# Performance work log

Hardware: AMD Instinct MI355X
Metric: run time of the kernel (lower is better)

The kernel has to match this reference:

```python
import jax, jax.numpy as jnp
import numpy as np

B, T, C = 2, 2048, 1024
NH = 16
HS = C // NH

def setup_inputs() -> dict:
    key = jax.random.key(0)
    ks = jax.random.split(key, 5)
    x = jax.random.normal(ks[0], (B, T, C), dtype=jnp.float32)
    scale = 1.0 / np.sqrt(C)
    Wk = jax.random.normal(ks[1], (C, C), dtype=jnp.float32) * scale
    bk = jax.random.normal(ks[2], (C,), dtype=jnp.float32) * scale
    Wv = jax.random.normal(ks[3], (C, C), dtype=jnp.float32) * scale
    bv = jax.random.normal(ks[4], (C,), dtype=jnp.float32) * scale
    return {"x": x, "Wk": Wk, "bk": bk, "Wv": Wv, "bv": bv}

def reference(x, Wk, bk, Wv, bv):
    b, t, c = x.shape
    # projections: key and value are Dense; query is identity (as in source)
    k = (x @ Wk + bk).reshape(b, t, NH, HS).transpose(0, 2, 1, 3)  # b nh T hs
    q = x.reshape(b, t, NH, HS).transpose(0, 2, 1, 3)              # b nh T hs
    v = (x @ Wv + bv).reshape(b, t, NH, HS).transpose(0, 2, 1, 3)  # b nh T hs
    # NOTE: source computes logits = K @ Q^T (no 1/sqrt(d) scaling)
    logits = jnp.einsum('bhid,bhjd->bhij', k, q)                   # b nh T T
    causal = jnp.tril(jnp.ones((t, t), dtype=bool))                # True where allowed
    masked = jnp.where(causal[None, None, :, :], logits, -jnp.inf)
    att = jax.nn.softmax(masked, axis=-1)
    y = jnp.einsum('bhij,bhjd->bhid', att, v)                      # b nh T hs
    return y.transpose(0, 2, 1, 3).reshape(b, t, c)
```

## Files before the change

kernel.cpp:

```cpp
#include <hip/hip_runtime.h>
#include <cstdint>
#include <cstddef>

#define BB  2
#define TT  2048
#define CC  1024
#define NHH 16
#define HSS 64
#define BT  (BB*TT)

#define LOG2E 1.44269504088896f
#define S0INIT (-28.8539008f)

typedef unsigned short u16;
typedef unsigned int u32;
typedef __attribute__((ext_vector_type(2))) unsigned int u32x2;
typedef _Float16 f16;
typedef __attribute__((ext_vector_type(8))) _Float16 f16x8;
typedef __attribute__((ext_vector_type(8))) __bf16 bf16x8;
typedef __attribute__((ext_vector_type(4))) float f32x4;

__device__ __forceinline__ u16 f2bf(float f) {
    union { float f; u32 u; } x; x.f = f;
    return (u16)((x.u + 0x7fffu + ((x.u >> 16) & 1u)) >> 16);
}
__device__ __forceinline__ u16 f2h(float f) {
    union { f16 h; u16 u; } x; x.h = (f16)f;
    return x.u;
}
__device__ __forceinline__ u32 cvtpk_bf16(float lo, float hi) {
    u32 r;
    asm("v_cvt_pk_bf16_f32 %0, %1, %2" : "=v"(r) : "v"(lo), "v"(hi));
    return r;
}

#define MFMA_BF(a,b,c) __builtin_amdgcn_mfma_f32_16x16x32_bf16((a),(b),(c),0,0,0)
#define MFMA_F16(a,b,c) __builtin_amdgcn_mfma_f32_16x16x32_f16((a),(b),(c),0,0,0)

__device__ __forceinline__ void gld16(const u16* g, u16* l) {
    __builtin_amdgcn_global_load_lds(
        (const __attribute__((address_space(1))) unsigned int*)g,
        (__attribute__((address_space(3))) unsigned int*)l, 16, 0, 0);
}

__global__ __launch_bounds__(256) void convert_xw(
    const float* __restrict__ X, const float* __restrict__ Wk,
    const float* __restrict__ Wv, u16* __restrict__ Xf,
    u16* __restrict__ WkT, u16* __restrict__ WvT)
{
    __shared__ __align__(16) u16 LH[64][72];
    const int bid = blockIdx.x;
    const int tid = threadIdx.x;
    if (bid < 2048) {
        const int idx = (bid * 256 + tid) * 8;
        const float4 a = *(const float4*)&X[idx];
        const float4 b = *(const float4*)&X[idx + 4];
        float v[8] = {a.x, a.y, a.z, a.w, b.x, b.y, b.z, b.w};
        union { uint4 u; u16 s[8]; } H;
        #pragma unroll
        for (int u = 0; u < 8; ++u) H.s[u] = f2h(v[u]);
        *(uint4*)&Xf[idx] = H.u;
        return;
    }
    const int bid2 = bid - 2048;
    const bool isK = (bid2 >> 8) == 0;
    const int rem = bid2 & 255;
    const int n0 = (rem & 15) * 64, k0 = (rem >> 4) * 64;
    const float* W = isK ? Wk : Wv;
    u16* WT = isK ? WkT : WvT;
    {
        const int row = tid >> 2, coff = (tid & 3) * 16;
        const float* g = &W[(size_t)(k0 + row) * CC + n0 + coff];
        #pragma unroll
        for (int u = 0; u < 16; ++u) LH[row][coff + u] = f2h(g[u]);
    }
    __syncthreads();
    {
        const int n = tid >> 2, kc = (tid & 3) * 16;
        union { uint4 u[2]; u16 s[16]; } Hq;
        #pragma unroll
        for (int u = 0; u < 16; ++u) Hq.s[u] = LH[kc + u][n];
        uint4* ph = (uint4*)&WT[(size_t)(n0 + n) * CC + k0 + kc];
        ph[0] = Hq.u[0]; ph[1] = Hq.u[1];
    }
}

__global__ __launch_bounds__(256) void proj_kernel(
    const u16* __restrict__ Xf, const u16* __restrict__ WkT,
    const u16* __restrict__ WvT,
    const float* __restrict__ bk, const float* __restrict__ bv,
    u16* __restrict__ Kf, u16* __restrict__ Vt)
{
    __shared__ __align__(16) u16 SM[4][8192];

    const int id = blockIdx.x;
    const int xcd = id & 7;
    const int z = xcd >> 2, xcd4 = xcd & 3;
    const int idx = id >> 3;
    const int n0 = (idx & 7) * 128;
    const int m0 = (xcd4 * 8 + (idx >> 3)) * 128;
    const bool isK = (z == 0);
    const u16* WT = isK ? WkT : WvT;

    const int tid = threadIdx.x;
    const int w = tid >> 6, lane = tid & 63;
    const int quad = lane >> 4, l15 = lane & 15;
    const int wm = (w >> 1) * 64, wn = (w & 1) * 64;

    const u16* src = (w < 2) ? Xf : WT;
    const int rbase = (w < 2) ? m0 : n0;
    int srow[4], scg[4];
    #pragma unroll
    for (int t = 0; t < 4; ++t) {
        const int ci = (w & 1) * 256 + t * 64 + lane;
        const int r = ci >> 2;
        srow[t] = r;
        scg[t] = ((ci & 3) - r - (r >> 2)) & 3;
    }
    const int dhalf = ((w >= 2) ? 4096 : 0) + (w & 1) * 2048;
    const u16* gsrc[4];
    #pragma unroll
    for (int t = 0; t < 4; ++t)
        gsrc[t] = src + (size_t)(rbase + srow[t]) * CC + scg[t] * 8;

    const char* smb = (const char*)&SM[0][0];
    int aoff[4], boff[4];
    #pragma unroll
    for (int i = 0; i < 4; ++i) {
        const int r = wm + i * 16 + l15;
        aoff[i] = r * 64 + ((quad + r + (r >> 2)) & 3) * 16;
    }
    #pragma unroll
    for (int j = 0; j < 4; ++j) {
        const int r = wn + j * 16 + l15;
        boff[j] = 8192 + r * 64 + ((quad + r + (r >> 2)) & 3) * 16;
    }

    f32x4 acc[4][4] = {};

#define PSTAGE(K, BI)                                                   \
    { u16* dst = &SM[BI][dhalf];                                        \
      _Pragma("unroll")                                                 \
      for (int t = 0; t < 4; ++t)                                       \
          gld16(gsrc[t] + (K) * 32, dst + t * 512); }

    PSTAGE(0, 0);
    PSTAGE(1, 1);

    for (int ki = 0; ki < 32; ++ki) {
        const int buf = ki & 3;
        if (ki < 30) PSTAGE(ki + 2, (ki + 2) & 3);
        if (ki < 30)       asm volatile("s_waitcnt vmcnt(8)" ::: "memory");
        else if (ki == 30) asm volatile("s_waitcnt vmcnt(4)" ::: "memory");
        else               asm volatile("s_waitcnt vmcnt(0)" ::: "memory");
        __builtin_amdgcn_sched_barrier(0);
        __builtin_amdgcn_s_barrier();
        __builtin_amdgcn_sched_barrier(0);
        const char* pb = smb + buf * 16384;
        f16x8 ah[4];
        #pragma unroll
        for (int i = 0; i < 4; ++i) ah[i] = *(const f16x8*)(pb + aoff[i]);
        #pragma unroll
        for (int j = 0; j < 4; ++j) {
            f16x8 bh = *(const f16x8*)(pb + boff[j]);
            #pragma unroll
            for (int i = 0; i < 4; ++i)
                acc[i][j] = MFMA_F16(ah[i], bh, acc[i][j]);
        }
    }
#undef PSTAGE

    __syncthreads();
    u16* XL = &SM[0][0];

    if (isK) {
        #pragma unroll
        for (int j = 0; j < 4; ++j) {
            const float bias = bk[n0 + wn + j * 16 + l15];
            #pragma unroll
            for (int i = 0; i < 4; ++i)
                #pragma unroll
                for (int r = 0; r < 4; ++r)
                    XL[(wm + i * 16 + quad * 4 + r) * 136 + wn + j * 16 + l15] =
                        f2h((acc[i][j][r] + bias) * LOG2E);
        }
        __syncthreads();
        const int r = tid >> 1, half = tid & 1;
        #pragma unroll
        for (int t = 0; t < 8; ++t)
            *(uint4*)&Kf[(size_t)(m0 + r) * CC + n0 + half * 64 + t * 8] =
                *(const uint4*)&XL[r * 136 + half * 64 + t * 8];
    } else {
        #pragma unroll
        for (int j = 0; j < 4; ++j) {
            const float bias = bv[n0 + wn + j * 16 + l15];
            #pragma unroll
            for (int i = 0; i < 4; ++i) {
                uint2 pk;
                pk.x = (u32)f2bf(acc[i][j][0] + bias) |
                       ((u32)f2bf(acc[i][j][1] + bias) << 16);
                pk.y = (u32)f2bf(acc[i][j][2] + bias) |
                       ((u32)f2bf(acc[i][j][3] + bias) << 16);
                *(uint2*)&XL[(wn + j * 16 + l15) * 136 + wm + i * 16 + quad * 4] = pk;
            }
        }
        __syncthreads();
        const int nl = tid >> 1, half = tid & 1;
        const int d = (n0 + nl) & (HSS - 1), hh = (n0 + nl) >> 6;
        const int bb = m0 >> 11, tb = (m0 & (TT - 1)) + half * 64;
        const size_t gb = ((size_t)(bb * NHH + hh) * HSS + d) * TT + tb;
        #pragma unroll
        for (int t = 0; t < 8; ++t)
            *(uint4*)&Vt[gb + t * 8] = *(const uint4*)&XL[nl * 136 + half * 64 + t * 8];
    }
}

__global__ __launch_bounds__(256) void attn_kernel(
    const u16* __restrict__ Xf, const u16* __restrict__ Kf,
    const u16* __restrict__ Vt, float* __restrict__ out)
{
    __shared__ __align__(16) u16 Xs[2][4096];
    __shared__ __align__(16) u16 Vs[2][4096];

    const int L = blockIdx.x;
    const int xcd = L & 7, k = (L >> 3) & 15, grp = L >> 7;
    const int hb = xcd + 8 * grp;
    const int h = hb & (NHH - 1), b = hb >> 4;
    const int iA = k, iB = 31 - k;
    const int i0A = iA * 64, i0B = iB * 64;

    const int tid = threadIdx.x;
    const int w = tid >> 6, lane = tid & 63;
    const int quad = lane >> 4, l15 = lane & 15;
    const int pq = ((quad & 1) << 1) | (quad >> 1);
    const size_t rowbase = (size_t)b * TT;
    const int hd = h * HSS;
    const size_t vgbase = (size_t)(b * NHH + h) * HSS * TT;

    bf16x8 ones;
    { union { u32 u[4]; bf16x8 v; } o;
      #pragma unroll
      for (int i = 0; i < 4; ++i) o.u[i] = 0x3F803F80u;
      ones = o.v; }

    f16x8 qA[2], qB[2];
    #pragma unroll
    for (int c = 0; c < 2; ++c) {
        qA[c] = *(const f16x8*)&Kf[(rowbase + i0A + w * 16 + l15) * CC + hd + c * 32 + quad * 8];
        qB[c] = *(const f16x8*)&Kf[(rowbase + i0B + w * 16 + l15) * CC + hd + c * 32 + quad * 8];
    }

    int crow[2], ccg[2], cbase[2];
    #pragma unroll
    for (int t = 0; t < 2; ++t) {
        const int ci = t * 256 + tid;
        crow[t] = ci >> 3;
        ccg[t] = ((ci & 7) - crow[t]) & 7;
        cbase[t] = (t * 256 + w * 64) * 8;
    }
    const u16* gx[2]; const u16* gv[2];
    #pragma unroll
    for (int t = 0; t < 2; ++t) {
        gx[t] = Xf + (rowbase + crow[t]) * CC + hd + ccg[t] * 8;
        gv[t] = Vt + vgbase + (size_t)crow[t] * TT + ccg[t] * 8;
    }

    #pragma unroll
    for (int t = 0; t < 2; ++t) {
        gld16(gx[t], Xs[0] + cbase[t]);
        gld16(gv[t], Vs[0] + cbase[t]);
    }

    f32x4 oA[4] = {}, oB[4] = {};
    f32x4 laA = {}, laB = {};

    for (int jt = 0; jt <= iB; ++jt) {
        const int buf = jt & 1;
        __syncthreads();
        if (jt < iB) {
            const int j0n = (jt + 1) * 64;
            #pragma unroll
            for (int t = 0; t < 2; ++t) {
                gld16(gx[t] + (size_t)j0n * CC, Xs[buf ^ 1] + cbase[t]);
                gld16(gv[t] + j0n, Vs[buf ^ 1] + cbase[t]);
            }
        }
        const bool doA = (jt <= iA);

        f32x4 sB[4], sA[4];
        #pragma unroll
        for (int nt = 0; nt < 4; ++nt) {
            const int krow = nt * 16 + l15;
            f16x8 x0 = *(const f16x8*)&Xs[buf][krow * 64 + ((quad + krow) & 7) * 8];
            f16x8 x1 = *(const f16x8*)&Xs[buf][krow * 64 + ((quad + 4 + krow) & 7) * 8];
            f32x4 z = {S0INIT, S0INIT, S0INIT, S0INIT};
            z = MFMA_F16(x0, qB[0], z);
            z = MFMA_F16(x1, qB[1], z);
            sB[nt] = z;
            if (doA) {
                f32x4 y = {S0INIT, S0INIT, S0INIT, S0INIT};
                y = MFMA_F16(x0, qA[0], y);
                y = MFMA_F16(x1, qA[1], y);
                sA[nt] = y;
            }
        }
        if (jt == iB) {
            #pragma unroll
            for (int nt = 0; nt < 4; ++nt)
                #pragma unroll
                for (int r = 0; r < 4; ++r)
                    if (nt * 16 + quad * 4 + r > w * 16 + l15) sB[nt][r] = -1e30f;
        }
        if (doA && jt == iA) {
            #pragma unroll
            for (int nt = 0; nt < 4; ++nt)
                #pragma unroll
                for (int r = 0; r < 4; ++r)
                    if (nt * 16 + quad * 4 + r > w * 16 + l15) sA[nt][r] = -1e30f;
        }

        u32 pB_[4][2];
        #pragma unroll
        for (int nt = 0; nt < 4; ++nt) {
            pB_[nt][0] = cvtpk_bf16(exp2f(sB[nt][0]), exp2f(sB[nt][1]));
            pB_[nt][1] = cvtpk_bf16(exp2f(sB[nt][2]), exp2f(sB[nt][3]));
        }
        #pragma unroll
        for (int c = 0; c < 2; ++c)
            #pragma unroll
            for (int p = 0; p < 2; ++p) {
                u32x2 sw = __builtin_amdgcn_permlane16_swap(
                    pB_[2 * c][p], pB_[2 * c + 1][p], false, false);
                pB_[2 * c][p] = sw[0];
                pB_[2 * c + 1][p] = sw[1];
            }
        union { u32 u[4]; bf16x8 v; } ub0, ub1;
        ub0.u[0] = pB_[0][0]; ub0.u[1] = pB_[0][1];
        ub0.u[2] = pB_[1][0]; ub0.u[3] = pB_[1][1];
        ub1.u[0] = pB_[2][0]; ub1.u[1] = pB_[2][1];
        ub1.u[2] = pB_[3][0]; ub1.u[3] = pB_[3][1];
        bf16x8 aB0 = ub0.v, aB1 = ub1.v;

        bf16x8 aA0, aA1;
        if (doA) {
            u32 pA_[4][2];
            #pragma unroll
            for (int nt = 0; nt < 4; ++nt) {
                pA_[nt][0] = cvtpk_bf16(exp2f(sA[nt][0]), exp2f(sA[nt][1]));
                pA_[nt][1] = cvtpk_bf16(exp2f(sA[nt][2]), exp2f(sA[nt][3]));
            }
            #pragma unroll
            for (int c = 0; c < 2; ++c)
                #pragma unroll
                for (int p = 0; p < 2; ++p) {
                    u32x2 sw = __builtin_amdgcn_permlane16_swap(
                        pA_[2 * c][p], pA_[2 * c + 1][p], false, false);
                    pA_[2 * c][p] = sw[0];
                    pA_[2 * c + 1][p] = sw[1];
                }
            union { u32 u[4]; bf16x8 v; } ua0, ua1;
            ua0.u[0] = pA_[0][0]; ua0.u[1] = pA_[0][1];
            ua0.u[2] = pA_[1][0]; ua0.u[3] = pA_[1][1];
            ua1.u[0] = pA_[2][0]; ua1.u[1] = pA_[2][1];
            ua1.u[2] = pA_[3][0]; ua1.u[3] = pA_[3][1];
            aA0 = ua0.v; aA1 = ua1.v;
        }

        laB = MFMA_BF(aB0, ones, laB);
        laB = MFMA_BF(aB1, ones, laB);
        if (doA) {
            laA = MFMA_BF(aA0, ones, laA);
            laA = MFMA_BF(aA1, ones, laA);
        }

        #pragma unroll
        for (int dt = 0; dt < 4; ++dt) {
            const int vrow = dt * 16 + l15;
            bf16x8 v0 = *(const bf16x8*)&Vs[buf][vrow * 64 + ((pq + vrow) & 7) * 8];
            bf16x8 v1 = *(const bf16x8*)&Vs[buf][vrow * 64 + ((pq + 4 + vrow) & 7) * 8];
            oB[dt] = MFMA_BF(aB0, v0, oB[dt]);
            oB[dt] = MFMA_BF(aB1, v1, oB[dt]);
            if (doA) {
                oA[dt] = MFMA_BF(aA0, v0, oA[dt]);
                oA[dt] = MFMA_BF(aA1, v1, oA[dt]);
            }
        }
    }

    float liA[4], liB[4];
    #pragma unroll
    for (int r = 0; r < 4; ++r) { liA[r] = 1.f / laA[r]; liB[r] = 1.f / laB[r]; }
    #pragma unroll
    for (int dt = 0; dt < 4; ++dt) {
        #pragma unroll
        for (int r = 0; r < 4; ++r) {
            const int igA = i0A + w * 16 + quad * 4 + r;
            const int igB = i0B + w * 16 + quad * 4 + r;
            out[(rowbase + igA) * CC + hd + dt * 16 + l15] = oA[dt][r] * liA[r];
            out[(rowbase + igB) * CC + hd + dt * 16 + l15] = oB[dt][r] * liB[r];
        }
    }
}

extern "C" void kernel_launch(void* const* d_in, const int* in_sizes, int n_in,
                              void* d_out, int out_size, void* d_ws, size_t ws_size,
                              hipStream_t stream) {
    (void)in_sizes; (void)n_in; (void)out_size; (void)ws_size;
    const float* x  = (const float*)d_in[0];
    const float* Wk = (const float*)d_in[1];
    const float* bk = (const float*)d_in[2];
    const float* Wv = (const float*)d_in[3];
    const float* bv = (const float*)d_in[4];
    float* out = (float*)d_out;

    const size_t M4 = (size_t)BT * CC;
    const size_t M1 = (size_t)CC * CC;
    u16* Xf  = (u16*)d_ws;
    u16* Kf  = Xf + M4;
    u16* Vt  = Kf + M4;
    u16* WkT = Vt + M4;
    u16* WvT = WkT + M1;

    convert_xw<<<dim3(2560), 256, 0, stream>>>(x, Wk, Wv, Xf, WkT, WvT);
    proj_kernel<<<dim3(512), 256, 0, stream>>>(Xf, WkT, WvT, bk, bv, Kf, Vt);
    attn_kernel<<<dim3(512), 256, 0, stream>>>(Xf, Kf, Vt, out);
}
```

Measured before the change: 154.2 us.

## Load K/V tiles directly from global into registers, dropping LDS double buffering

```diff
diff --git a/kernel.cpp b/kernel.cpp
--- a/kernel.cpp
+++ b/kernel.cpp
@@ -219,9 +219,6 @@
     const u16* __restrict__ Xf, const u16* __restrict__ Kf,
     const u16* __restrict__ Vt, float* __restrict__ out)
 {
-    __shared__ __align__(16) u16 Xs[2][4096];
-    __shared__ __align__(16) u16 Vs[2][4096];
-
     const int L = blockIdx.x;
     const int xcd = L & 7, k = (L >> 3) & 15, grp = L >> 7;
     const int hb = xcd + 8 * grp;
@@ -250,57 +247,46 @@
         qB[c] = *(const f16x8*)&Kf[(rowbase + i0B + w * 16 + l15) * CC + hd + c * 32 + quad * 8];
     }
 
-    int crow[2], ccg[2], cbase[2];
-    #pragma unroll
-    for (int t = 0; t < 2; ++t) {
-        const int ci = t * 256 + tid;
-        crow[t] = ci >> 3;
-        ccg[t] = ((ci & 7) - crow[t]) & 7;
-        cbase[t] = (t * 256 + w * 64) * 8;
-    }
-    const u16* gx[2]; const u16* gv[2];
-    #pragma unroll
-    for (int t = 0; t < 2; ++t) {
-        gx[t] = Xf + (rowbase + crow[t]) * CC + hd + ccg[t] * 8;
-        gv[t] = Vt + vgbase + (size_t)crow[t] * TT + ccg[t] * 8;
-    }
-
-    #pragma unroll
-    for (int t = 0; t < 2; ++t) {
-        gld16(gx[t], Xs[0] + cbase[t]);
-        gld16(gv[t], Vs[0] + cbase[t]);
+    const u16* xr[4];
+    const u16* vr[4];
+    #pragma unroll
+    for (int t = 0; t < 4; ++t) {
+        xr[t] = Xf + (rowbase + t * 16 + l15) * CC + hd + quad * 8;
+        vr[t] = Vt + vgbase + (size_t)(t * 16 + l15) * TT + pq * 8;
     }
 
     f32x4 oA[4] = {}, oB[4] = {};
     f32x4 laA = {}, laB = {};
 
     for (int jt = 0; jt <= iB; ++jt) {
-        const int buf = jt & 1;
-        __syncthreads();
-        if (jt < iB) {
-            const int j0n = (jt + 1) * 64;
-            #pragma unroll
-            for (int t = 0; t < 2; ++t) {
-                gld16(gx[t] + (size_t)j0n * CC, Xs[buf ^ 1] + cbase[t]);
-                gld16(gv[t] + j0n, Vs[buf ^ 1] + cbase[t]);
-            }
-        }
         const bool doA = (jt <= iA);
 
+        f16x8 x0[4], x1[4];
+        bf16x8 v0[4], v1[4];
+        #pragma unroll
+        for (int t = 0; t < 4; ++t) {
+            x0[t] = *(const f16x8*)(xr[t]);
+            x1[t] = *(const f16x8*)(xr[t] + 32);
+            v0[t] = *(const bf16x8*)(vr[t]);
+            v1[t] = *(const bf16x8*)(vr[t] + 32);
+        }
+        #pragma unroll
+        for (int t = 0; t < 4; ++t) {
+            xr[t] += 64 * CC;
+            vr[t] += 64;
+        }
+
         f32x4 sB[4], sA[4];
         #pragma unroll
         for (int nt = 0; nt < 4; ++nt) {
-            const int krow = nt * 16 + l15;
-            f16x8 x0 = *(const f16x8*)&Xs[buf][krow * 64 + ((quad + krow) & 7) * 8];
-            f16x8 x1 = *(const f16x8*)&Xs[buf][krow * 64 + ((quad + 4 + krow) & 7) * 8];
             f32x4 z = {S0INIT, S0INIT, S0INIT, S0INIT};
-            z = MFMA_F16(x0, qB[0], z);
-            z = MFMA_F16(x1, qB[1], z);
+            z = MFMA_F16(x0[nt], qB[0], z);
+            z = MFMA_F16(x1[nt], qB[1], z);
             sB[nt] = z;
             if (doA) {
                 f32x4 y = {S0INIT, S0INIT, S0INIT, S0INIT};
-                y = MFMA_F16(x0, qA[0], y);
-                y = MFMA_F16(x1, qA[1], y);
+                y = MFMA_F16(x0[nt], qA[0], y);
+                y = MFMA_F16(x1[nt], qA[1], y);
                 sA[nt] = y;
             }
         }
@@ -375,14 +361,11 @@
 
         #pragma unroll
         for (int dt = 0; dt < 4; ++dt) {
-            const int vrow = dt * 16 + l15;
-            bf16x8 v0 = *(const bf16x8*)&Vs[buf][vrow * 64 + ((pq + vrow) & 7) * 8];
-            bf16x8 v1 = *(const bf16x8*)&Vs[buf][vrow * 64 + ((pq + 4 + vrow) & 7) * 8];
-            oB[dt] = MFMA_BF(aB0, v0, oB[dt]);
-            oB[dt] = MFMA_BF(aB1, v1, oB[dt]);
+            oB[dt] = MFMA_BF(aB0, v0[dt], oB[dt]);
+            oB[dt] = MFMA_BF(aB1, v1[dt], oB[dt]);
             if (doA) {
-                oA[dt] = MFMA_BF(aA0, v0, oA[dt]);
-                oA[dt] = MFMA_BF(aA1, v1, oA[dt]);
+                oA[dt] = MFMA_BF(aA0, v0[dt], oA[dt]);
+                oA[dt] = MFMA_BF(aA1, v1[dt], oA[dt]);
             }
         }
     }
```

Result: slower. 222.1 us (+44.0%).

## Deepen attention K/V prefetch to 4-buffer, 2-ahead pipeline with explicit vmcnt waits

Applied to the files above, without the earlier changes.

```diff
diff --git a/kernel.cpp b/kernel.cpp
--- a/kernel.cpp
+++ b/kernel.cpp
@@ -219,8 +219,8 @@
     const u16* __restrict__ Xf, const u16* __restrict__ Kf,
     const u16* __restrict__ Vt, float* __restrict__ out)
 {
-    __shared__ __align__(16) u16 Xs[2][4096];
-    __shared__ __align__(16) u16 Vs[2][4096];
+    __shared__ __align__(16) u16 Xs[4][4096];
+    __shared__ __align__(16) u16 Vs[4][4096];
 
     const int L = blockIdx.x;
     const int xcd = L & 7, k = (L >> 3) & 15, grp = L >> 7;
@@ -265,26 +265,34 @@
         gv[t] = Vt + vgbase + (size_t)crow[t] * TT + ccg[t] * 8;
     }
 
-    #pragma unroll
-    for (int t = 0; t < 2; ++t) {
-        gld16(gx[t], Xs[0] + cbase[t]);
-        gld16(gv[t], Vs[0] + cbase[t]);
-    }
+#define ASTAGE(JT, BI)                                                  \
+    { const int j0_ = (JT) * 64;                                        \
+      _Pragma("unroll")                                                 \
+      for (int t = 0; t < 2; ++t) {                                     \
+          gld16(gx[t] + (size_t)j0_ * CC, Xs[BI] + cbase[t]);           \
+          gld16(gv[t] + j0_, Vs[BI] + cbase[t]);                        \
+      } }
+
+    ASTAGE(0, 0);
+    ASTAGE(1, 1);
 
     f32x4 oA[4] = {}, oB[4] = {};
     f32x4 laA = {}, laB = {};
 
     for (int jt = 0; jt <= iB; ++jt) {
-        const int buf = jt & 1;
-        __syncthreads();
-        if (jt < iB) {
-            const int j0n = (jt + 1) * 64;
-            #pragma unroll
-            for (int t = 0; t < 2; ++t) {
-                gld16(gx[t] + (size_t)j0n * CC, Xs[buf ^ 1] + cbase[t]);
-                gld16(gv[t] + j0n, Vs[buf ^ 1] + cbase[t]);
-            }
-        }
+        const int buf = jt & 3;
+        if (jt + 2 <= iB) {
+            ASTAGE(jt + 2, (jt + 2) & 3);
+            asm volatile("s_waitcnt vmcnt(8)" ::: "memory");
+        } else if (jt + 1 <= iB) {
+            asm volatile("s_waitcnt vmcnt(4)" ::: "memory");
+        } else {
+            asm volatile("s_waitcnt vmcnt(0)" ::: "memory");
+        }
+        __builtin_amdgcn_sched_barrier(0);
+        __builtin_amdgcn_s_barrier();
+        __builtin_amdgcn_sched_barrier(0);
+
         const bool doA = (jt <= iA);
 
         f32x4 sB[4], sA[4];
@@ -386,6 +394,7 @@
             }
         }
     }
+#undef ASTAGE
 
     float liA[4], liB[4];
     #pragma unroll
```

Result: no change. 155.6 us (+0.9%).

## Split attention work across warps by query tile and key half with LDS reduction

Applied to the files above, without the earlier changes.

```diff
diff --git a/kernel.cpp b/kernel.cpp
--- a/kernel.cpp
+++ b/kernel.cpp
@@ -221,16 +221,20 @@
 {
     __shared__ __align__(16) u16 Xs[2][4096];
     __shared__ __align__(16) u16 Vs[2][4096];
+    __shared__ float OL[2][64][65];
+    __shared__ float Ll[2][64];
 
     const int L = blockIdx.x;
     const int xcd = L & 7, k = (L >> 3) & 15, grp = L >> 7;
     const int hb = xcd + 8 * grp;
     const int h = hb & (NHH - 1), b = hb >> 4;
     const int iA = k, iB = 31 - k;
-    const int i0A = iA * 64, i0B = iB * 64;
-
     const int tid = threadIdx.x;
     const int w = tid >> 6, lane = tid & 63;
+    const int T = w >> 1;
+    const int H = w & 1;
+    const int iT = T ? iB : iA;
+    const int i0T = iT * 64;
     const int quad = lane >> 4, l15 = lane & 15;
     const int pq = ((quad & 1) << 1) | (quad >> 1);
     const size_t rowbase = (size_t)b * TT;
@@ -243,12 +247,13 @@
       for (int i = 0; i < 4; ++i) o.u[i] = 0x3F803F80u;
       ones = o.v; }
 
-    f16x8 qA[2], qB[2];
-    #pragma unroll
-    for (int c = 0; c < 2; ++c) {
-        qA[c] = *(const f16x8*)&Kf[(rowbase + i0A + w * 16 + l15) * CC + hd + c * 32 + quad * 8];
-        qB[c] = *(const f16x8*)&Kf[(rowbase + i0B + w * 16 + l15) * CC + hd + c * 32 + quad * 8];
-    }
+    f16x8 q[4][2];
+    #pragma unroll
+    for (int iq = 0; iq < 4; ++iq)
+        #pragma unroll
+        for (int c = 0; c < 2; ++c)
+            q[iq][c] = *(const f16x8*)&Kf[(rowbase + i0T + iq * 16 + l15) * CC +
+                                          hd + c * 32 + quad * 8];
 
     int crow[2], ccg[2], cbase[2];
     #pragma unroll
@@ -271,8 +276,8 @@
         gld16(gv[t], Vs[0] + cbase[t]);
     }
 
-    f32x4 oA[4] = {}, oB[4] = {};
-    f32x4 laA = {}, laB = {};
+    f32x4 o[4][4] = {};
+    f32x4 la[4] = {};
 
     for (int jt = 0; jt <= iB; ++jt) {
         const int buf = jt & 1;
@@ -285,119 +290,94 @@
                 gld16(gv[t] + j0n, Vs[buf ^ 1] + cbase[t]);
             }
         }
-        const bool doA = (jt <= iA);
-
-        f32x4 sB[4], sA[4];
-        #pragma unroll
-        for (int nt = 0; nt < 4; ++nt) {
-            const int krow = nt * 16 + l15;
-            f16x8 x0 = *(const f16x8*)&Xs[buf][krow * 64 + ((quad + krow) & 7) * 8];
-            f16x8 x1 = *(const f16x8*)&Xs[buf][krow * 64 + ((quad + 4 + krow) & 7) * 8];
-            f32x4 z = {S0INIT, S0INIT, S0INIT, S0INIT};
-            z = MFMA_F16(x0, qB[0], z);
-            z = MFMA_F16(x1, qB[1], z);
-            sB[nt] = z;
-            if (doA) {
-                f32x4 y = {S0INIT, S0INIT, S0INIT, S0INIT};
-                y = MFMA_F16(x0, qA[0], y);
-                y = MFMA_F16(x1, qA[1], y);
-                sA[nt] = y;
-            }
-        }
-        if (jt == iB) {
-            #pragma unroll
-            for (int nt = 0; nt < 4; ++nt)
+        if (jt > iT) continue;
+
+        f16x8 x[2][2];
+        #pragma unroll
+        for (int nt2 = 0; nt2 < 2; ++nt2) {
+            const int krow = H * 32 + nt2 * 16 + l15;
+            x[nt2][0] = *(const f16x8*)&Xs[buf][krow * 64 + ((quad + krow) & 7) * 8];
+            x[nt2][1] = *(const f16x8*)&Xs[buf][krow * 64 + ((quad + 4 + krow) & 7) * 8];
+        }
+        bf16x8 v[4];
+        #pragma unroll
+        for (int dt = 0; dt < 4; ++dt) {
+            const int vrow = dt * 16 + l15;
+            v[dt] = *(const bf16x8*)&Vs[buf][vrow * 64 + ((H * 4 + pq + vrow) & 7) * 8];
+        }
+
+        const bool diag = (jt == iT);
+        #pragma unroll
+        for (int iq = 0; iq < 4; ++iq) {
+            f32x4 s[2];
+            #pragma unroll
+            for (int nt2 = 0; nt2 < 2; ++nt2) {
+                f32x4 z = {S0INIT, S0INIT, S0INIT, S0INIT};
+                z = MFMA_F16(x[nt2][0], q[iq][0], z);
+                z = MFMA_F16(x[nt2][1], q[iq][1], z);
+                s[nt2] = z;
+            }
+            if (diag) {
                 #pragma unroll
-                for (int r = 0; r < 4; ++r)
-                    if (nt * 16 + quad * 4 + r > w * 16 + l15) sB[nt][r] = -1e30f;
-        }
-        if (doA && jt == iA) {
-            #pragma unroll
-            for (int nt = 0; nt < 4; ++nt)
-                #pragma unroll
-                for (int r = 0; r < 4; ++r)
-                    if (nt * 16 + quad * 4 + r > w * 16 + l15) sA[nt][r] = -1e30f;
-        }
-
-        u32 pB_[4][2];
-        #pragma unroll
-        for (int nt = 0; nt < 4; ++nt) {
-            pB_[nt][0] = cvtpk_bf16(exp2f(sB[nt][0]), exp2f(sB[nt][1]));
-            pB_[nt][1] = cvtpk_bf16(exp2f(sB[nt][2]), exp2f(sB[nt][3]));
-        }
-        #pragma unroll
-        for (int c = 0; c < 2; ++c)
+                for (int nt2 = 0; nt2 < 2; ++nt2)
+                    #pragma unroll
+                    for (int r = 0; r < 4; ++r)
+                        if (H * 32 + nt2 * 16 + quad * 4 + r > iq * 16 + l15)
+                            s[nt2][r] = -1e30f;
+            }
+            u32 p_[2][2];
+            #pragma unroll
+            for (int nt2 = 0; nt2 < 2; ++nt2) {
+                p_[nt2][0] = cvtpk_bf16(exp2f(s[nt2][0]), exp2f(s[nt2][1]));
+                p_[nt2][1] = cvtpk_bf16(exp2f(s[nt2][2]), exp2f(s[nt2][3]));
+            }
             #pragma unroll
             for (int p = 0; p < 2; ++p) {
                 u32x2 sw = __builtin_amdgcn_permlane16_swap(
-                    pB_[2 * c][p], pB_[2 * c + 1][p], false, false);
-                pB_[2 * c][p] = sw[0];
-                pB_[2 * c + 1][p] = sw[1];
-            }
-        union { u32 u[4]; bf16x8 v; } ub0, ub1;
-        ub0.u[0] = pB_[0][0]; ub0.u[1] = pB_[0][1];
-        ub0.u[2] = pB_[1][0]; ub0.u[3] = pB_[1][1];
-        ub1.u[0] = pB_[2][0]; ub1.u[1] = pB_[2][1];
-        ub1.u[2] = pB_[3][0]; ub1.u[3] = pB_[3][1];
-        bf16x8 aB0 = ub0.v, aB1 = ub1.v;
-
-        bf16x8 aA0, aA1;
-        if (doA) {
-            u32 pA_[4][2];
-            #pragma unroll
-            for (int nt = 0; nt < 4; ++nt) {
-                pA_[nt][0] = cvtpk_bf16(exp2f(sA[nt][0]), exp2f(sA[nt][1]));
-                pA_[nt][1] = cvtpk_bf16(exp2f(sA[nt][2]), exp2f(sA[nt][3]));
-            }
-            #pragma unroll
-            for (int c = 0; c < 2; ++c)
+                    p_[0][p], p_[1][p], false, false);
+                p_[0][p] = sw[0];
+                p_[1][p] = sw[1];
+            }
+            union { u32 u[4]; bf16x8 vv; } ua;
+            ua.u[0] = p_[0][0]; ua.u[1] = p_[0][1];
+            ua.u[2] = p_[1][0]; ua.u[3] = p_[1][1];
+            const bf16x8 a = ua.vv;
+
+            la[iq] = MFMA_BF(a, ones, la[iq]);
+            #pragma unroll
+            for (int dt = 0; dt < 4; ++dt)
+                o[iq][dt] = MFMA_BF(a, v[dt], o[iq][dt]);
+        }
+    }
+
+    __syncthreads();
+    if (H == 1) {
+        #pragma unroll
+        for (int iq = 0; iq < 4; ++iq) {
+            #pragma unroll
+            for (int r = 0; r < 4; ++r) {
+                const int il = iq * 16 + quad * 4 + r;
+                if (l15 == 0) Ll[T][il] = la[iq][r];
                 #pragma unroll
-                for (int p = 0; p < 2; ++p) {
-                    u32x2 sw = __builtin_amdgcn_permlane16_swap(
-                        pA_[2 * c][p], pA_[2 * c + 1][p], false, false);
-                    pA_[2 * c][p] = sw[0];
-                    pA_[2 * c + 1][p] = sw[1];
-                }
-            union { u32 u[4]; bf16x8 v; } ua0, ua1;
-            ua0.u[0] = pA_[0][0]; ua0.u[1] = pA_[0][1];
-            ua0.u[2] = pA_[1][0]; ua0.u[3] = pA_[1][1];
-            ua1.u[0] = pA_[2][0]; ua1.u[1] = pA_[2][1];
-            ua1.u[2] = pA_[3][0]; ua1.u[3] = pA_[3][1];
-            aA0 = ua0.v; aA1 = ua1.v;
-        }
-
-        laB = MFMA_BF(aB0, ones, laB);
-        laB = MFMA_BF(aB1, ones, laB);
-        if (doA) {
-            laA = MFMA_BF(aA0, ones, laA);
-            laA = MFMA_BF(aA1, ones, laA);
-        }
-
-        #pragma unroll
-        for (int dt = 0; dt < 4; ++dt) {
-            const int vrow = dt * 16 + l15;
-            bf16x8 v0 = *(const bf16x8*)&Vs[buf][vrow * 64 + ((pq + vrow) & 7) * 8];
-            bf16x8 v1 = *(const bf16x8*)&Vs[buf][vrow * 64 + ((pq + 4 + vrow) & 7) * 8];
-            oB[dt] = MFMA_BF(aB0, v0, oB[dt]);
-            oB[dt] = MFMA_BF(aB1, v1, oB[dt]);
-            if (doA) {
-                oA[dt] = MFMA_BF(aA0, v0, oA[dt]);
-                oA[dt] = MFMA_BF(aA1, v1, oA[dt]);
-            }
-        }
-    }
-
-    float liA[4], liB[4];
-    #pragma unroll
-    for (int r = 0; r < 4; ++r) { liA[r] = 1.f / laA[r]; liB[r] = 1.f / laB[r]; }
-    #pragma unroll
-    for (int dt = 0; dt < 4; ++dt) {
-        #pragma unroll
-        for (int r = 0; r < 4; ++r) {
-            const int igA = i0A + w * 16 + quad * 4 + r;
-            const int igB = i0B + w * 16 + quad * 4 + r;
-            out[(rowbase + igA) * CC + hd + dt * 16 + l15] = oA[dt][r] * liA[r];
-            out[(rowbase + igB) * CC + hd + dt * 16 + l15] = oB[dt][r] * liB[r];
+                for (int dt = 0; dt < 4; ++dt)
+                    OL[T][il][dt * 16 + l15] = o[iq][dt][r];
+            }
+        }
+    }
+    __syncthreads();
+    if (H == 0) {
+        #pragma unroll
+        for (int iq = 0; iq < 4; ++iq) {
+            #pragma unroll
+            for (int r = 0; r < 4; ++r) {
+                const int il = iq * 16 + quad * 4 + r;
+                const float inv = 1.f / (la[iq][r] + Ll[T][il]);
+                const size_t rowoff = (rowbase + i0T + il) * CC + hd;
+                #pragma unroll
+                for (int dt = 0; dt < 4; ++dt)
+                    out[rowoff + dt * 16 + l15] =
+                        (o[iq][dt][r] + OL[T][il][dt * 16 + l15]) * inv;
+            }
         }
     }
 }
```

After: 171.0 us. +10.8%, slower.
